# Performance work log

Hardware: AMD Instinct MI355X
Metric: run time of the kernel (lower is better)

The kernel has to match this reference:

```python
import jax, jax.numpy as jnp
import numpy as np

ND, PD, NH = 256, 128, 8   # node_dim, pair_dim, n_head
HD = ND // NH              # head_dim = 32
N, L = 1, 256


def _inorm(x):
    # InstanceNorm2d (affine=False), x is NHWC: normalize per (N,C) over H,W
    m = jnp.mean(x, axis=(1, 2), keepdims=True)
    v = jnp.var(x, axis=(1, 2), keepdims=True)
    return (x - m) * jax.lax.rsqrt(v + 1e-5)


def _conv3x3(x, w, b):
    # w in torch OIHW layout -> HWIO; stride 1, padding 1 ('SAME')
    y = jax.lax.conv_general_dilated(x, jnp.transpose(w, (2, 3, 1, 0)), (1, 1), 'SAME',
                                     dimension_numbers=('NHWC', 'HWIO', 'NHWC'))
    return y + b


def _lrelu(x):
    return jnp.where(x >= 0, x, 0.01 * x)


def _ln(x, g, b):
    m = jnp.mean(x, axis=-1, keepdims=True)
    v = jnp.var(x, axis=-1, keepdims=True)
    return (x - m) * jax.lax.rsqrt(v + 1e-5) * g + b


def setup_inputs() -> dict:
    key = jax.random.key(0)
    ks = jax.random.split(key, 16)
    rn = lambda k, s: jax.random.normal(k, s, jnp.float32) * 0.02
    return dict(
        x=jax.random.normal(ks[0], (N, L, ND), jnp.float32),
        z=jax.random.normal(ks[1], (N, L, L, PD), jnp.float32),
        plddt=jax.random.uniform(ks[2], (N, L, L, 1), jnp.float32),
        Wq=rn(ks[3], (ND, ND)), Wk=rn(ks[4], (ND, ND)), Wv=rn(ks[5], (ND, ND)),
        Wp2a=rn(ks[6], (NH, PD)),
        conv_a_w=rn(ks[7], (NH, 2 * NH, 3, 3)), conv_a_b=jnp.zeros((NH,), jnp.float32),
        conv_p_w=rn(ks[8], (NH, NH + 1, 3, 3)), conv_p_b=jnp.zeros((NH,), jnp.float32),
        ln1_g=jnp.ones((NH * PD + ND,), jnp.float32), ln1_b=jnp.zeros((NH * PD + ND,), jnp.float32),
        lin1_w=rn(ks[9], (2 * ND, NH * PD + ND)), lin1_b=jnp.zeros((2 * ND,), jnp.float32),
        ln2_g=jnp.ones((2 * ND,), jnp.float32), ln2_b=jnp.zeros((2 * ND,), jnp.float32),
        lin2_w=rn(ks[10], (ND, 2 * ND)), lin2_b=jnp.zeros((ND,), jnp.float32),
        lnf_g=jnp.ones((ND,), jnp.float32), lnf_b=jnp.zeros((ND,), jnp.float32),
        conv_z_w=rn(ks[11], (PD, NH + PD, 3, 3)), conv_z_b=jnp.zeros((PD,), jnp.float32),
    )


def reference(x, z, plddt, Wq, Wk, Wv, Wp2a, conv_a_w, conv_a_b, conv_p_w, conv_p_b,
              ln1_g, ln1_b, lin1_w, lin1_b, ln2_g, ln2_b, lin2_w, lin2_b,
              lnf_g, lnf_b, conv_z_w, conv_z_b):
    n, l, _ = x.shape
    inv_sqrt_hd = np.float32(1.0 / np.sqrt(HD))
    # _node2alpha: per-head QK^T / sqrt(head_dim) -> (N,L,L,H)
    q = (x @ Wq.T).reshape(n, l, NH, HD)
    k = (x @ Wk.T).reshape(n, l, NH, HD)
    v = (x @ Wv.T).reshape(n, l, NH, HD)
    a_node = jnp.einsum('nihd,njhd->nijh', q, k) * inv_sqrt_hd
    # _pair2alpha
    a_pair = z @ Wp2a.T  # (N,L,L,H)
    # conv2dalpha: cat(pair, node) channels-last, InstanceNorm + Conv3x3 + LeakyReLU
    alpha = _lrelu(_conv3x3(_inorm(jnp.concatenate([a_pair, a_node], axis=-1)), conv_a_w, conv_a_b))
    # alpha_mask_plddt
    alpha = _lrelu(_conv3x3(_inorm(jnp.concatenate([alpha, plddt], axis=-1)), conv_p_w, conv_p_b))
    # _node_aggregation: (N,L,H,hd) head-major flatten -> (N,L,node_dim)
    node_from_node = jnp.einsum('nijh,njhd->nihd', alpha, v).reshape(n, l, ND)
    # _pair_aggregation: direct contraction over j (avoids (N,L,L,H,P) blowup)
    node_from_pair = jnp.einsum('nijh,nijp->nihp', alpha, z).reshape(n, l, NH * PD)
    # out_transform: LN -> Linear -> LN -> LeakyReLU -> Linear
    h = jnp.concatenate([node_from_pair, node_from_node], axis=-1)
    h = _ln(h, ln1_g, ln1_b)
    h = _ln(h @ lin1_w.T + lin1_b, ln2_g, ln2_b)
    x_out = _lrelu(h) @ lin2_w.T + lin2_b
    x_new = _ln(x + x_out, lnf_g, lnf_b)
    # alpha2pair
    z_new = _lrelu(_conv3x3(_inorm(jnp.concatenate([z, alpha], axis=-1)), conv_z_w, conv_z_b))
    return x_new, z_new
```

## Files before the change

### kernel.cpp

```cpp
#include <hip/hip_runtime.h>
#include <math.h>

#define LLEN 256
#define NDIM 256
#define NHEAD 8
#define HDIM 32
#define NPIX (LLEN*LLEN)

typedef __bf16 bf16x8 __attribute__((ext_vector_type(8)));
typedef float f32x4 __attribute__((ext_vector_type(4)));

constexpr size_t OFF_Q     = 0;
constexpr size_t OFF_K     = 65536;
constexpr size_t OFF_V     = 131072;
constexpr size_t OFF_CAT16 = 196608;
constexpr size_t OFF_H1B   = 196608;
constexpr size_t OFF_W1B   = 360448;
constexpr size_t OFF_A1    = 1245184;
constexpr size_t OFF_ALPHA = 1769472;
constexpr size_t OFF_AGG   = 2293760;
constexpr size_t OFF_Y     = 2621440;
constexpr size_t OFF_ST16  = 2752512;
constexpr size_t OFF_ST9   = 2752544;
constexpr size_t OFF_ST136 = 2752576;
constexpr size_t OFF_PART  = 2752864;
constexpr size_t OFF_PART2 = 2892128;
constexpr size_t OFF_WZB2  = 3031392;

__device__ inline unsigned short f2b(float x){
  union { float f; unsigned u; } a; a.f = x;
  unsigned r = a.u + 0x7fffu + ((a.u >> 16) & 1u);
  return (unsigned short)(r >> 16);
}

__global__ __launch_bounds__(256) void qkv2_kernel(
    const float* __restrict__ x, const float* __restrict__ Wq,
    const float* __restrict__ Wk, const float* __restrict__ Wv,
    float* __restrict__ q, float* __restrict__ k, float* __restrict__ v){
  __shared__ __align__(16) float xs[4][256];
  int t = threadIdx.x;
  int i0 = blockIdx.x * 4;
  int m = blockIdx.y;
  const float* W = (m==0)?Wq:((m==1)?Wk:Wv);
  float* out = (m==0)?q:((m==1)?k:v);
  for (int idx = t; idx < 1024; idx += 256)
    xs[idx>>8][idx&255] = x[(size_t)i0*256 + idx];
  __syncthreads();
  float acc[4];
  #pragma unroll
  for (int r = 0; r < 4; r++) acc[r] = 0.f;
  const float4* wr = (const float4*)(W + (size_t)t*256);
  for (int kk = 0; kk < 64; ++kk){
    float4 w4 = wr[kk];
    #pragma unroll
    for (int r = 0; r < 4; r++){
      float4 xv = ((const float4*)xs[r])[kk];
      acc[r] += w4.x*xv.x + w4.y*xv.y + w4.z*xv.z + w4.w*xv.w;
    }
  }
  #pragma unroll
  for (int r = 0; r < 4; r++) out[(size_t)(i0+r)*256 + t] = acc[r];
}

__global__ __launch_bounds__(256) void cat16v5_kernel(
    const float* __restrict__ z, const float* __restrict__ qb,
    const float* __restrict__ kb, const float* __restrict__ Wp2a,
    float* __restrict__ cat16, float* __restrict__ p16, float* __restrict__ p16q,
    float* __restrict__ zpart, float* __restrict__ zpartq){
  __shared__ __align__(16) float zs2[32*132];
  __shared__ __align__(16) float ws2[8*132];
  __shared__ float sA[512];
  int t = threadIdx.x;
  int pix0 = blockIdx.x * 32;
  int i = pix0 >> 8;
  int j0 = pix0 & 255;
  { int h = t >> 5, j = t & 31;
    float4 v = *(const float4*)(Wp2a + h*128 + j*4);
    *(float4*)(ws2 + h*132 + j*4) = v; }
  #pragma unroll
  for (int k = 0; k < 4; ++k){
    int idx = t + k*256;
    int pix = idx >> 5, j = idx & 31;
    float4 v = *(const float4*)(z + ((size_t)(pix0 + pix))*128 + j*4);
    *(float4*)(zs2 + pix*132 + j*4) = v;
  }
  __syncthreads();
  int p8 = t >> 3, h = t & 7;
  const float* zr = zs2 + p8*132;
  const float* wr = ws2 + h*132;
  float ap = 0.f;
  #pragma unroll 8
  for (int j = 0; j < 32; ++j){
    float4 a = *(const float4*)(zr + j*4);
    float4 b = *(const float4*)(wr + j*4);
    ap += a.x*b.x + a.y*b.y + a.z*b.z + a.w*b.w;
  }
  const float* qg = qb + (size_t)i*256 + h*32;
  const float* kg = kb + (size_t)(j0 + p8)*256 + h*32;
  float an = 0.f;
  #pragma unroll
  for (int d4 = 0; d4 < 8; ++d4){
    float4 a = *(const float4*)(qg + d4*4);
    float4 b = *(const float4*)(kg + d4*4);
    an += a.x*b.x + a.y*b.y + a.z*b.z + a.w*b.w;
  }
  an *= 0.17677669529663689f;
  int pix = pix0 + p8;
  cat16[(size_t)pix*16 + h] = ap;
  cat16[(size_t)pix*16 + 8 + h] = an;
  sA[p8*16 + h] = ap;
  sA[p8*16 + 8 + h] = an;
  __syncthreads();
  if (t < 16){
    float S = 0.f, Q = 0.f;
    #pragma unroll
    for (int p = 0; p < 32; ++p){ float v = sA[p*16 + t]; S += v; Q += v*v; }
    p16 [(size_t)t*2048 + blockIdx.x] = S;
    p16q[(size_t)t*2048 + blockIdx.x] = Q;
  }
  if (t < 128){
    float S = 0.f, Q = 0.f;
    #pragma unroll 8
    for (int p = 0; p < 32; ++p){ float v = zs2[p*132 + t]; S += v; Q += v*v; }
    zpart [(size_t)t*2048 + blockIdx.x] = S;
    zpartq[(size_t)t*2048 + blockIdx.x] = Q;
  }
}

__device__ inline void block_reduce2(float& s, float& s2, float* red){
  int t = threadIdx.x;
  int lane = t & 63, wv = t >> 6;
  #pragma unroll
  for (int o = 32; o > 0; o >>= 1){ s += __shfl_down(s, o); s2 += __shfl_down(s2, o); }
  __syncthreads();
  if (lane == 0){ red[wv] = s; red[4+wv] = s2; }
  __syncthreads();
  s  = red[0]+red[1]+red[2]+red[3];
  s2 = red[4]+red[5]+red[6]+red[7];
}

__device__ inline void block_reduce2_512(float& s, float& s2, float* red16){
  int t = threadIdx.x;
  int lane = t & 63, wv = t >> 6;
  #pragma unroll
  for (int o = 32; o > 0; o >>= 1){ s += __shfl_down(s, o); s2 += __shfl_down(s2, o); }
  __syncthreads();
  if (lane == 0){ red16[wv] = s; red16[8+wv] = s2; }
  __syncthreads();
  s = 0.f; s2 = 0.f;
  #pragma unroll
  for (int j = 0; j < 8; ++j){ s += red16[j]; s2 += red16[8+j]; }
}

__global__ __launch_bounds__(256) void statsB_kernel(
    const float* __restrict__ part, const float* __restrict__ part2,
    float* __restrict__ st, int C, int co, int nb, int stride){
  __shared__ float red[8];
  int c = blockIdx.x, t = threadIdx.x;
  float s = 0.f, q = 0.f;
  for (int i = t; i < nb; i += 256){
    s += part[(size_t)c*stride + i];
    q += part2[(size_t)c*stride + i];
  }
  block_reduce2(s, q, red);
  if (t == 0){
    float m = s * (1.f/NPIX);
    float var = q * (1.f/NPIX) - m*m;
    st[co + c] = m;
    st[C + co + c] = rsqrtf(var + 1e-5f);
  }
}

__global__ __launch_bounds__(256) void statsB2_kernel(
    const float* __restrict__ p16, const float* __restrict__ p16q,
    float* __restrict__ st16,
    const float* __restrict__ zpart, const float* __restrict__ zpartq,
    float* __restrict__ st136){
  __shared__ float red[8];
  int b = blockIdx.x, t = threadIdx.x;
  const float* P; const float* Q; float* st; int C, c;
  if (b < 16){ P = p16; Q = p16q; st = st16; C = 16; c = b; }
  else       { P = zpart; Q = zpartq; st = st136; C = 136; c = b - 16; }
  float s = 0.f, q = 0.f;
  for (int i = t; i < 2048; i += 256){
    s += P[(size_t)c*2048 + i];
    q += Q[(size_t)c*2048 + i];
  }
  block_reduce2(s, q, red);
  if (t == 0){
    float m = s * (1.f/NPIX);
    float var = q * (1.f/NPIX) - m*m;
    st[c] = m;
    st[C + c] = rsqrtf(var + 1e-5f);
  }
}

template<int CIN, int COUT, bool PL>
__global__ __launch_bounds__(256) void conv_small6_kernel(
    const float* __restrict__ A, int Ca, const float* __restrict__ B, int Cb,
    const float* __restrict__ st, const float* __restrict__ w,
    const float* __restrict__ bias, float* __restrict__ out,
    const float* __restrict__ plddt, float* __restrict__ part,
    float* __restrict__ part2, int coff){
  constexpr int WD = 67;
  __shared__ float xn[3][CIN][WD];
  __shared__ float wsm[COUT*CIN*9];
  __shared__ float ms[CIN], isd[CIN], bs[COUT];
  __shared__ float sB[COUT*64];
  __shared__ float sP[64];
  int t = threadIdx.x;
  int i = blockIdx.x >> 2, chb = blockIdx.x & 3;
  int c0 = chb*64;
  if (t < CIN){ ms[t] = st[t]; isd[t] = st[CIN + t]; }
  if (t < COUT) bs[t] = bias[t];
  for (int idx = t; idx < COUT*CIN*9; idx += 256) wsm[idx] = w[idx];
  __syncthreads();
  constexpr int TOT = 66*CIN;
  for (int s = 0; s < 3; ++s){
    int ir = i - 1 + s;
    for (int idx = t; idx < TOT; idx += 256){
      int col = idx / CIN, c = idx - col*CIN;
      int gcol = c0 + col - 1;
      float vv = 0.f;
      if (ir >= 0 && ir < 256 && gcol >= 0 && gcol < 256){
        size_t pix = (size_t)ir*256 + gcol;
        float raw = (c < Ca) ? A[pix*Ca + c] : B[pix*Cb + (c - Ca)];
        vv = (raw - ms[c]) * isd[c];
      }
      xn[s][c][col] = vv;
    }
  }
  __syncthreads();
  int os = t >> 6, tc = t & 63;
  float a0 = bs[os*2], a1 = bs[os*2 + 1];
  #pragma unroll
  for (int kh = 0; kh < 3; ++kh){
    #pragma unroll
    for (int c = 0; c < CIN; ++c){
      float x0 = xn[kh][c][tc];
      float x1 = xn[kh][c][tc + 1];
      float x2 = xn[kh][c][tc + 2];
      const float* w0 = wsm + (((os*2+0)*CIN + c)*3 + kh)*3;
      const float* w1 = wsm + (((os*2+1)*CIN + c)*3 + kh)*3;
      a0 += x0*w0[0] + x1*w0[1] + x2*w0[2];
      a1 += x0*w1[0] + x1*w1[1] + x2*w1[2];
    }
  }
  a0 = (a0 >= 0.f) ? a0 : 0.01f*a0;
  a1 = (a1 >= 0.f) ? a1 : 0.01f*a1;
  float2 v2 = { a0, a1 };
  *(float2*)(out + ((size_t)(i*256 + c0 + tc))*COUT + os*2) = v2;
  sB[os*128 + tc]      = a0;
  sB[os*128 + 64 + tc] = a1;
  if (PL && t < 64) sP[t] = plddt[(size_t)i*256 + c0 + t];
  __syncthreads();
  if (t < COUT){
    int os2 = t >> 1, par = t & 1;
    const float* src = sB + os2*128 + par*64;
    float S = 0.f, Q = 0.f;
    #pragma unroll
    for (int j = 0; j < 64; ++j){ float v = src[j]; S += v; Q += v*v; }
    part [(size_t)(coff + t)*1024 + blockIdx.x] = S;
    part2[(size_t)(coff + t)*1024 + blockIdx.x] = Q;
  } else if (PL && t == COUT){
    float S = 0.f, Q = 0.f;
    #pragma unroll
    for (int j = 0; j < 64; ++j){ float v = sP[j]; S += v; Q += v*v; }
    part [(size_t)(coff + COUT)*1024 + blockIdx.x] = S;
    part2[(size_t)(coff + COUT)*1024 + blockIdx.x] = Q;
  }
}

__global__ __launch_bounds__(512) void agg_ln1_kernel(
    const float* __restrict__ alpha, const float* __restrict__ z,
    const float* __restrict__ v,
    const float* __restrict__ ln1_g, const float* __restrict__ ln1_b,
    unsigned short* __restrict__ h1b){
  __shared__ float as[2048];
  __shared__ float pp[256][4];
  __shared__ float np[256];
  __shared__ float red16[16];
  int i = blockIdx.x, t = threadIdx.x;
  for (int idx = t; idx < 2048; idx += 512) as[idx] = alpha[(size_t)i*2048 + idx];
  __syncthreads();
  int tt = t & 255, jh = t >> 8;
  int p = tt & 127, hh = tt >> 7;
  const float* zrow = z + (size_t)i*32768 + (size_t)jh*128*128;
  const float* ar0 = as + jh*128*8;
  float a0=0.f, a1=0.f, a2=0.f, a3=0.f;
  #pragma unroll 8
  for (int j = 0; j < 128; ++j){
    float zv = zrow[j*128 + p];
    const float* ar = ar0 + j*8 + hh*4;
    a0 += ar[0]*zv; a1 += ar[1]*zv; a2 += ar[2]*zv; a3 += ar[3]*zv;
  }
  int h = tt >> 5;
  float an = 0.f;
  const float* vrow = v + (size_t)jh*128*256;
  const float* ah0 = as + jh*128*8;
  #pragma unroll 8
  for (int j = 0; j < 128; ++j) an += ah0[j*8 + h]*vrow[j*256 + tt];
  if (jh == 1){
    pp[tt][0]=a0; pp[tt][1]=a1; pp[tt][2]=a2; pp[tt][3]=a3; np[tt]=an;
  }
  __syncthreads();
  float s = 0.f, s2 = 0.f;
  if (jh == 0){
    a0 += pp[tt][0]; a1 += pp[tt][1]; a2 += pp[tt][2]; a3 += pp[tt][3];
    an += np[tt];
    s  = a0 + a1 + a2 + a3 + an;
    s2 = a0*a0 + a1*a1 + a2*a2 + a3*a3 + an*an;
  }
  block_reduce2_512(s, s2, red16);
  float m = s*(1.f/1280.f), istd = rsqrtf(s2*(1.f/1280.f) - m*m + 1e-5f);
  if (jh == 0){
    size_t ob = (size_t)i*1280;
    int k0 = (hh*4+0)*128 + p;
    int k1 = (hh*4+1)*128 + p;
    int k2 = (hh*4+2)*128 + p;
    int k3 = (hh*4+3)*128 + p;
    int k4 = 1024 + tt;
    h1b[ob + k0] = f2b((a0 - m)*istd*ln1_g[k0] + ln1_b[k0]);
    h1b[ob + k1] = f2b((a1 - m)*istd*ln1_g[k1] + ln1_b[k1]);
    h1b[ob + k2] = f2b((a2 - m)*istd*ln1_g[k2] + ln1_b[k2]);
    h1b[ob + k3] = f2b((a3 - m)*istd*ln1_g[k3] + ln1_b[k3]);
    h1b[ob + k4] = f2b((an - m)*istd*ln1_g[k4] + ln1_b[k4]);
  }
}

__global__ __launch_bounds__(256) void prep_kernel(
    const float* __restrict__ lw, unsigned short* __restrict__ wb,
    const float* __restrict__ zw, unsigned short* __restrict__ wzb2){
  int bid = blockIdx.x;
  if (bid < 640){
    int idx = (bid*256 + threadIdx.x)*4;
    float4 v = *(const float4*)(lw + idx);
    ushort4 u;
    u.x = f2b(v.x); u.y = f2b(v.y); u.z = f2b(v.z); u.w = f2b(v.w);
    *(ushort4*)(wb + idx) = u;
  } else {
    int idx = (bid - 640)*256 + threadIdx.x;
    if (idx < 23040){
      int lane = idx & 63;
      int f = idx >> 6;
      int k = f % 5; int ft = f / 5; int tap = ft % 9; int ocb = ft / 9;
      int oc = ocb*16 + (lane & 15);
      int chb = k*32 + (lane >> 4)*8;
      unsigned short u[8];
      #pragma unroll
      for (int j = 0; j < 8; ++j){
        int ch = chb + j;
        float vv = (ch < 136) ? zw[(size_t)oc*1224 + ch*9 + tap] : 0.f;
        u[j] = f2b(vv);
      }
      uint4 pk;
      pk.x = (unsigned)u[0] | ((unsigned)u[1]<<16);
      pk.y = (unsigned)u[2] | ((unsigned)u[3]<<16);
      pk.z = (unsigned)u[4] | ((unsigned)u[5]<<16);
      pk.w = (unsigned)u[6] | ((unsigned)u[7]<<16);
      *(uint4*)(wzb2 + (size_t)idx*8) = pk;
    }
  }
}

__global__ __launch_bounds__(256) void gemm1_kernel(
    const unsigned short* __restrict__ h1b, const unsigned short* __restrict__ w1b,
    const float* __restrict__ lin1_b, float* __restrict__ y){
  int t = threadIdx.x;
  int mb = blockIdx.x & 3, nb = blockIdx.x >> 2;
  int lane = t & 63, w = t >> 6;
  int li = lane & 15, lg = lane >> 4;
  int mh = w & 1, nh = w >> 1;
  int mbase = mb*64 + mh*32, nbase = nb*64 + nh*32;
  f32x4 acc[2][2];
  #pragma unroll
  for (int a = 0; a < 2; ++a)
    #pragma unroll
    for (int b = 0; b < 2; ++b) acc[a][b] = (f32x4){0.f,0.f,0.f,0.f};
  const unsigned short* ar0 = h1b + (size_t)(mbase + li)*1280 + lg*8;
  const unsigned short* ar1 = ar0 + 16*1280;
  const unsigned short* br0 = w1b + (size_t)(nbase + li)*1280 + lg*8;
  const unsigned short* br1 = br0 + 16*1280;
  #pragma unroll 4
  for (int ks = 0; ks < 40; ++ks){
    bf16x8 a0 = *(const bf16x8*)(ar0 + ks*32);
    bf16x8 a1 = *(const bf16x8*)(ar1 + ks*32);
    bf16x8 b0 = *(const bf16x8*)(br0 + ks*32);
    bf16x8 b1 = *(const bf16x8*)(br1 + ks*32);
    acc[0][0] = __builtin_amdgcn_mfma_f32_16x16x32_bf16(a0, b0, acc[0][0], 0,0,0);
    acc[0][1] = __builtin_amdgcn_mfma_f32_16x16x32_bf16(a0, b1, acc[0][1], 0,0,0);
    acc[1][0] = __builtin_amdgcn_mfma_f32_16x16x32_bf16(a1, b0, acc[1][0], 0,0,0);
    acc[1][1] = __builtin_amdgcn_mfma_f32_16x16x32_bf16(a1, b1, acc[1][1], 0,0,0);
  }
  #pragma unroll
  for (int mi = 0; mi < 2; ++mi){
    #pragma unroll
    for (int ni = 0; ni < 2; ++ni){
      int col = nbase + ni*16 + li;
      float bb = lin1_b[col];
      #pragma unroll
      for (int ri = 0; ri < 4; ++ri){
        int row = mbase + mi*16 + lg*4 + ri;
        y[(size_t)row*512 + col] = acc[mi][ni][ri] + bb;
      }
    }
  }
}

__global__ __launch_bounds__(256) void outB2_kernel(
    const float* __restrict__ y, const float* __restrict__ x,
    const float* __restrict__ ln2_g, const float* __restrict__ ln2_b,
    const float* __restrict__ lin2_w, const float* __restrict__ lin2_b,
    const float* __restrict__ lnf_g, const float* __restrict__ lnf_b,
    float* __restrict__ xout){
  __shared__ __align__(16) float h2[2][512];
  __shared__ float red[8];
  int t = threadIdx.x;
  int rb = blockIdx.x;
  for (int r = 0; r < 2; ++r){
    int i = rb*2 + r;
    float y0 = y[(size_t)i*512 + t], y1 = y[(size_t)i*512 + 256 + t];
    float s = y0 + y1, s2 = y0*y0 + y1*y1;
    block_reduce2(s, s2, red);
    float m = s*(1.f/512.f), istd = rsqrtf(s2*(1.f/512.f) - m*m + 1e-5f);
    float z0 = (y0 - m)*istd*ln2_g[t] + ln2_b[t];
    float z1 = (y1 - m)*istd*ln2_g[t+256] + ln2_b[t+256];
    h2[r][t]     = (z0 >= 0.f) ? z0 : 0.01f*z0;
    h2[r][t+256] = (z1 >= 0.f) ? z1 : 0.01f*z1;
  }
  __syncthreads();
  float acc[2];
  acc[0] = 0.f; acc[1] = 0.f;
  const float4* wr = (const float4*)(lin2_w + (size_t)t*512);
  #pragma unroll 4
  for (int kk = 0; kk < 128; ++kk){
    float4 w4 = wr[kk];
    #pragma unroll
    for (int r = 0; r < 2; ++r){
      float4 h = ((const float4*)h2[r])[kk];
      acc[r] += w4.x*h.x + w4.y*h.y + w4.z*h.z + w4.w*h.w;
    }
  }
  float bb = lin2_b[t];
  for (int r = 0; r < 2; ++r){
    int i = rb*2 + r;
    float xr = x[(size_t)i*256 + t] + acc[r] + bb;
    float s = xr, s2 = xr*xr;
    block_reduce2(s, s2, red);
    float m = s*(1.f/256.f), istd = rsqrtf(s2*(1.f/256.f) - m*m + 1e-5f);
    xout[(size_t)i*256 + t] = (xr - m)*istd*lnf_g[t] + lnf_b[t];
  }
}

__global__ __launch_bounds__(256) void conv_z7_kernel(
    const float* __restrict__ z, const float* __restrict__ alpha,
    const float* __restrict__ st, const unsigned short* __restrict__ wzb2,
    const float* __restrict__ bias, float* __restrict__ out){
  __shared__ __align__(16) unsigned short xs[4*578*8];
  __shared__ float msp[153], isp[153];
  int t = threadIdx.x;
  int stripe = blockIdx.x & 7, rg = blockIdx.x >> 3;
  int i0 = rg*2, c0 = stripe*32;
  int lane = t & 63, w = t >> 6;
  int li = lane & 15, lg = lane >> 4;
  int wocb = w*2;
  if (t < 153){
    int cq = t/9, j = t - cq*9;
    bool vld = (j < 8);
    int ch = cq*8 + j;
    msp[t] = vld ? st[ch] : 0.f;
    isp[t] = vld ? st[136 + ch] : 0.f;
  }
  __syncthreads();
  for (int it = 0; it < 3; ++it){
    int cidx = t + it*256;
    int col = cidx / 17, cq = cidx - col*17;
    int gcol = c0 + col - 1;
    float mm[8], ss[8];
    #pragma unroll
    for (int j = 0; j < 8; ++j){ mm[j] = msp[cq*9 + j]; ss[j] = isp[cq*9 + j]; }
    if (cidx < 578){
      #pragma unroll
      for (int s = 0; s < 4; ++s){
        int ir = i0 - 1 + s;
        uint4 pk = {0u,0u,0u,0u};
        if (ir >= 0 && ir < 256 && gcol >= 0 && gcol < 256){
          const float* src = (cq < 16) ? (z + ((size_t)ir*256 + gcol)*128 + cq*8)
                                       : (alpha + ((size_t)ir*256 + gcol)*8);
          float4 r0 = *(const float4*)src;
          float4 r1 = *(const float4*)(src + 4);
          unsigned short u0 = f2b((r0.x - mm[0])*ss[0]);
          unsigned short u1 = f2b((r0.y - mm[1])*ss[1]);
          unsigned short u2 = f2b((r0.z - mm[2])*ss[2]);
          unsigned short u3 = f2b((r0.w - mm[3])*ss[3]);
          unsigned short u4 = f2b((r1.x - mm[4])*ss[4]);
          unsigned short u5 = f2b((r1.y - mm[5])*ss[5]);
          unsigned short u6 = f2b((r1.z - mm[6])*ss[6]);
          unsigned short u7 = f2b((r1.w - mm[7])*ss[7]);
          pk.x = (unsigned)u0 | ((unsigned)u1<<16);
          pk.y = (unsigned)u2 | ((unsigned)u3<<16);
          pk.z = (unsigned)u4 | ((unsigned)u5<<16);
          pk.w = (unsigned)u6 | ((unsigned)u7<<16);
        }
        *(uint4*)(xs + ((size_t)(s*578 + cidx))*8) = pk;
      }
    }
  }
  __syncthreads();

  f32x4 acc[2][2][2];
  #pragma unroll
  for (int r = 0; r < 2; ++r)
    #pragma unroll
    for (int m = 0; m < 2; ++m)
      #pragma unroll
      for (int o = 0; o < 2; ++o) acc[r][m][o] = (f32x4){0.f,0.f,0.f,0.f};

  for (int kh = 0; kh < 3; ++kh){
    for (int kw = 0; kw < 3; ++kw){
      int tap = kh*3 + kw;
      bf16x8 wf[5][2];
      #pragma unroll
      for (int k = 0; k < 5; ++k)
        #pragma unroll
        for (int o = 0; o < 2; ++o)
          wf[k][o] = *(const bf16x8*)(wzb2 + (size_t)((((wocb+o)*9 + tap)*5 + k)*64 + lane)*8);
      #pragma unroll
      for (int r = 0; r < 2; ++r){
        const unsigned short* sb = xs + (size_t)(r + kh)*578*8;
        #pragma unroll
        for (int k = 0; k < 5; ++k){
          int cq = (k < 4) ? (k*4 + lg) : 16;
          bf16x8 a0 = *(const bf16x8*)(sb + ((li+kw)*17 + cq)*8);
          bf16x8 a1 = *(const bf16x8*)(sb + ((li+kw+16)*17 + cq)*8);
          acc[r][0][0] = __builtin_amdgcn_mfma_f32_16x16x32_bf16(a0, wf[k][0], acc[r][0][0], 0,0,0);
          acc[r][0][1] = __builtin_amdgcn_mfma_f32_16x16x32_bf16(a0, wf[k][1], acc[r][0][1], 0,0,0);
          acc[r][1][0] = __builtin_amdgcn_mfma_f32_16x16x32_bf16(a1, wf[k][0], acc[r][1][0], 0,0,0);
          acc[r][1][1] = __builtin_amdgcn_mfma_f32_16x16x32_bf16(a1, wf[k][1], acc[r][1][1], 0,0,0);
        }
      }
    }
  }

  float b0 = bias[wocb*16 + li];
  float b1 = bias[(wocb+1)*16 + li];
  #pragma unroll
  for (int r = 0; r < 2; ++r){
    int i = i0 + r;
    #pragma unroll
    for (int m = 0; m < 2; ++m){
      #pragma unroll
      for (int ri = 0; ri < 4; ++ri){
        int px = m*16 + lg*4 + ri;
        size_t obase = ((size_t)(i*256 + c0 + px))*128;
        float v0 = acc[r][m][0][ri] + b0;
        float v1 = acc[r][m][1][ri] + b1;
        v0 = (v0 >= 0.f) ? v0 : 0.01f*v0;
        v1 = (v1 >= 0.f) ? v1 : 0.01f*v1;
        out[obase + wocb*16 + li]     = v0;
        out[obase + (wocb+1)*16 + li] = v1;
      }
    }
  }
}

extern "C" void kernel_launch(void* const* d_in, const int* in_sizes, int n_in,
                              void* d_out, int out_size, void* d_ws, size_t ws_size,
                              hipStream_t stream){
  const float* x        = (const float*)d_in[0];
  const float* z        = (const float*)d_in[1];
  const float* plddt    = (const float*)d_in[2];
  const float* Wq       = (const float*)d_in[3];
  const float* Wk       = (const float*)d_in[4];
  const float* Wv       = (const float*)d_in[5];
  const float* Wp2a     = (const float*)d_in[6];
  const float* conv_a_w = (const float*)d_in[7];
  const float* conv_a_b = (const float*)d_in[8];
  const float* conv_p_w = (const float*)d_in[9];
  const float* conv_p_b = (const float*)d_in[10];
  const float* ln1_g    = (const float*)d_in[11];
  const float* ln1_b    = (const float*)d_in[12];
  const float* lin1_w   = (const float*)d_in[13];
  const float* lin1_b   = (const float*)d_in[14];
  const float* ln2_g    = (const float*)d_in[15];
  const float* ln2_b    = (const float*)d_in[16];
  const float* lin2_w   = (const float*)d_in[17];
  const float* lin2_b   = (const float*)d_in[18];
  const float* lnf_g    = (const float*)d_in[19];
  const float* lnf_b    = (const float*)d_in[20];
  const float* conv_z_w = (const float*)d_in[21];
  const float* conv_z_b = (const float*)d_in[22];

  float* ws    = (float*)d_ws;
  float* q     = ws + OFF_Q;
  float* k     = ws + OFF_K;
  float* v     = ws + OFF_V;
  float* cat16 = ws + OFF_CAT16;
  float* a1    = ws + OFF_A1;
  float* zpart = ws + OFF_A1;
  float* zpartq= ws + OFF_A1 + 262144;
  float* alpha = ws + OFF_ALPHA;
  float* y     = ws + OFF_Y;
  float* p16   = ws + OFF_Y;
  float* p16q  = ws + OFF_Y + 32768;
  float* st16  = ws + OFF_ST16;
  float* st9   = ws + OFF_ST9;
  float* st136 = ws + OFF_ST136;
  float* part  = ws + OFF_PART;
  float* part2 = ws + OFF_PART2;
  unsigned short* wzb2 = (unsigned short*)(ws + OFF_WZB2);
  unsigned short* h1b  = (unsigned short*)(ws + OFF_H1B);
  unsigned short* w1b  = (unsigned short*)(ws + OFF_W1B);

  float* xout = (float*)d_out;
  float* zout = (float*)d_out + 65536;

  qkv2_kernel<<<dim3(64,3), 256, 0, stream>>>(x, Wq, Wk, Wv, q, k, v);
  cat16v5_kernel<<<2048, 256, 0, stream>>>(z, q, k, Wp2a, cat16, p16, p16q,
                                           zpart, zpartq);
  statsB2_kernel<<<144, 256, 0, stream>>>(p16, p16q, st16, zpart, zpartq, st136);
  conv_small6_kernel<16,8,true><<<1024, 256, 0, stream>>>(
      cat16, 16, (const float*)nullptr, 0, st16, conv_a_w, conv_a_b, a1,
      plddt, part, part2, 0);
  statsB_kernel<<<9, 256, 0, stream>>>(part, part2, st9, 9, 0, 1024, 1024);
  conv_small6_kernel<9,8,false><<<1024, 256, 0, stream>>>(
      a1, 8, plddt, 1, st9, conv_p_w, conv_p_b, alpha,
      (const float*)nullptr, part, part2, 128);
  statsB_kernel<<<8, 256, 0, stream>>>(part + (size_t)128*1024,
                                       part2 + (size_t)128*1024,
                                       st136, 136, 128, 1024, 1024);
  agg_ln1_kernel<<<256, 512, 0, stream>>>(alpha, z, v, ln1_g, ln1_b, h1b);
  prep_kernel<<<730, 256, 0, stream>>>(lin1_w, w1b, conv_z_w, wzb2);
  gemm1_kernel<<<32, 256, 0, stream>>>(h1b, w1b, lin1_b, y);
  outB2_kernel<<<128, 256, 0, stream>>>(y, x, ln2_g, ln2_b, lin2_w, lin2_b,
                                        lnf_g, lnf_b, xout);
  conv_z7_kernel<<<1024, 256, 0, stream>>>(z, alpha, st136, wzb2, conv_z_b, zout);
}
```

Measured before the change: 175.1 us.

## Fuse lin1 GEMM with LN2, lin2 and final LN into one kernel

```diff
diff --git a/kernel.cpp b/kernel.cpp
--- a/kernel.cpp
+++ b/kernel.cpp
@@ -18,7 +18,6 @@
 constexpr size_t OFF_W1B   = 360448;
 constexpr size_t OFF_A1    = 1245184;
 constexpr size_t OFF_ALPHA = 1769472;
-constexpr size_t OFF_AGG   = 2293760;
 constexpr size_t OFF_Y     = 2621440;
 constexpr size_t OFF_ST16  = 2752512;
 constexpr size_t OFF_ST9   = 2752544;
@@ -363,88 +362,73 @@
   }
 }
 
-__global__ __launch_bounds__(256) void gemm1_kernel(
+__global__ __launch_bounds__(256) void out_fused_kernel(
     const unsigned short* __restrict__ h1b, const unsigned short* __restrict__ w1b,
-    const float* __restrict__ lin1_b, float* __restrict__ y){
-  int t = threadIdx.x;
-  int mb = blockIdx.x & 3, nb = blockIdx.x >> 2;
-  int lane = t & 63, w = t >> 6;
-  int li = lane & 15, lg = lane >> 4;
-  int mh = w & 1, nh = w >> 1;
-  int mbase = mb*64 + mh*32, nbase = nb*64 + nh*32;
-  f32x4 acc[2][2];
-  #pragma unroll
-  for (int a = 0; a < 2; ++a)
-    #pragma unroll
-    for (int b = 0; b < 2; ++b) acc[a][b] = (f32x4){0.f,0.f,0.f,0.f};
-  const unsigned short* ar0 = h1b + (size_t)(mbase + li)*1280 + lg*8;
-  const unsigned short* ar1 = ar0 + 16*1280;
-  const unsigned short* br0 = w1b + (size_t)(nbase + li)*1280 + lg*8;
-  const unsigned short* br1 = br0 + 16*1280;
-  #pragma unroll 4
-  for (int ks = 0; ks < 40; ++ks){
-    bf16x8 a0 = *(const bf16x8*)(ar0 + ks*32);
-    bf16x8 a1 = *(const bf16x8*)(ar1 + ks*32);
-    bf16x8 b0 = *(const bf16x8*)(br0 + ks*32);
-    bf16x8 b1 = *(const bf16x8*)(br1 + ks*32);
-    acc[0][0] = __builtin_amdgcn_mfma_f32_16x16x32_bf16(a0, b0, acc[0][0], 0,0,0);
-    acc[0][1] = __builtin_amdgcn_mfma_f32_16x16x32_bf16(a0, b1, acc[0][1], 0,0,0);
-    acc[1][0] = __builtin_amdgcn_mfma_f32_16x16x32_bf16(a1, b0, acc[1][0], 0,0,0);
-    acc[1][1] = __builtin_amdgcn_mfma_f32_16x16x32_bf16(a1, b1, acc[1][1], 0,0,0);
-  }
-  #pragma unroll
-  for (int mi = 0; mi < 2; ++mi){
-    #pragma unroll
-    for (int ni = 0; ni < 2; ++ni){
-      int col = nbase + ni*16 + li;
-      float bb = lin1_b[col];
-      #pragma unroll
-      for (int ri = 0; ri < 4; ++ri){
-        int row = mbase + mi*16 + lg*4 + ri;
-        y[(size_t)row*512 + col] = acc[mi][ni][ri] + bb;
-      }
-    }
-  }
-}
-
-__global__ __launch_bounds__(256) void outB2_kernel(
-    const float* __restrict__ y, const float* __restrict__ x,
+    const float* __restrict__ lin1_b, const float* __restrict__ x,
     const float* __restrict__ ln2_g, const float* __restrict__ ln2_b,
     const float* __restrict__ lin2_w, const float* __restrict__ lin2_b,
     const float* __restrict__ lnf_g, const float* __restrict__ lnf_b,
     float* __restrict__ xout){
-  __shared__ __align__(16) float h2[2][512];
+  __shared__ __align__(16) float yl[8][512];
   __shared__ float red[8];
   int t = threadIdx.x;
-  int rb = blockIdx.x;
-  for (int r = 0; r < 2; ++r){
-    int i = rb*2 + r;
-    float y0 = y[(size_t)i*512 + t], y1 = y[(size_t)i*512 + 256 + t];
+  int i0 = blockIdx.x * 8;
+  int lane = t & 63, w = t >> 6;
+  int li = lane & 15, lg = lane >> 4;
+  int arow = i0 + li; if (arow > 255) arow = 255;
+  f32x4 acc[8];
+  #pragma unroll
+  for (int n = 0; n < 8; ++n) acc[n] = (f32x4){0.f,0.f,0.f,0.f};
+  const unsigned short* ar = h1b + (size_t)arow*1280 + lg*8;
+  #pragma unroll 4
+  for (int ks = 0; ks < 40; ++ks){
+    bf16x8 a = *(const bf16x8*)(ar + ks*32);
+    #pragma unroll
+    for (int n = 0; n < 8; ++n){
+      const unsigned short* br = w1b + (size_t)(w*128 + n*16 + li)*1280 + ks*32 + lg*8;
+      bf16x8 b = *(const bf16x8*)br;
+      acc[n] = __builtin_amdgcn_mfma_f32_16x16x32_bf16(a, b, acc[n], 0,0,0);
+    }
+  }
+  #pragma unroll
+  for (int n = 0; n < 8; ++n){
+    int col = w*128 + n*16 + li;
+    float bb = lin1_b[col];
+    #pragma unroll
+    for (int ri = 0; ri < 4; ++ri){
+      int dr = lg*4 + ri;
+      if (dr < 8) yl[dr][col] = acc[n][ri] + bb;
+    }
+  }
+  __syncthreads();
+  for (int r = 0; r < 8; ++r){
+    float y0 = yl[r][t], y1 = yl[r][t + 256];
     float s = y0 + y1, s2 = y0*y0 + y1*y1;
     block_reduce2(s, s2, red);
     float m = s*(1.f/512.f), istd = rsqrtf(s2*(1.f/512.f) - m*m + 1e-5f);
     float z0 = (y0 - m)*istd*ln2_g[t] + ln2_b[t];
     float z1 = (y1 - m)*istd*ln2_g[t+256] + ln2_b[t+256];
-    h2[r][t]     = (z0 >= 0.f) ? z0 : 0.01f*z0;
-    h2[r][t+256] = (z1 >= 0.f) ? z1 : 0.01f*z1;
-  }
-  __syncthreads();
-  float acc[2];
-  acc[0] = 0.f; acc[1] = 0.f;
-  const float4* wr = (const float4*)(lin2_w + (size_t)t*512);
+    yl[r][t]     = (z0 >= 0.f) ? z0 : 0.01f*z0;
+    yl[r][t+256] = (z1 >= 0.f) ? z1 : 0.01f*z1;
+    __syncthreads();
+  }
+  float a8[8];
+  #pragma unroll
+  for (int r = 0; r < 8; ++r) a8[r] = 0.f;
+  const float4* wr2 = (const float4*)(lin2_w + (size_t)t*512);
   #pragma unroll 4
   for (int kk = 0; kk < 128; ++kk){
-    float4 w4 = wr[kk];
-    #pragma unroll
-    for (int r = 0; r < 2; ++r){
-      float4 h = ((const float4*)h2[r])[kk];
-      acc[r] += w4.x*h.x + w4.y*h.y + w4.z*h.z + w4.w*h.w;
-    }
-  }
-  float bb = lin2_b[t];
-  for (int r = 0; r < 2; ++r){
-    int i = rb*2 + r;
-    float xr = x[(size_t)i*256 + t] + acc[r] + bb;
+    float4 w4 = wr2[kk];
+    #pragma unroll
+    for (int r = 0; r < 8; ++r){
+      float4 h = *(const float4*)(&yl[r][kk*4]);
+      a8[r] += w4.x*h.x + w4.y*h.y + w4.z*h.z + w4.w*h.w;
+    }
+  }
+  float bb2 = lin2_b[t];
+  for (int r = 0; r < 8; ++r){
+    int i = i0 + r;
+    float xr = x[(size_t)i*256 + t] + a8[r] + bb2;
     float s = xr, s2 = xr*xr;
     block_reduce2(s, s2, red);
     float m = s*(1.f/256.f), istd = rsqrtf(s2*(1.f/256.f) - m*m + 1e-5f);
@@ -600,7 +584,6 @@
   float* zpart = ws + OFF_A1;
   float* zpartq= ws + OFF_A1 + 262144;
   float* alpha = ws + OFF_ALPHA;
-  float* y     = ws + OFF_Y;
   float* p16   = ws + OFF_Y;
   float* p16q  = ws + OFF_Y + 32768;
   float* st16  = ws + OFF_ST16;
@@ -631,8 +614,8 @@
                                        st136, 136, 128, 1024, 1024);
   agg_ln1_kernel<<<256, 512, 0, stream>>>(alpha, z, v, ln1_g, ln1_b, h1b);
   prep_kernel<<<730, 256, 0, stream>>>(lin1_w, w1b, conv_z_w, wzb2);
-  gemm1_kernel<<<32, 256, 0, stream>>>(h1b, w1b, lin1_b, y);
-  outB2_kernel<<<128, 256, 0, stream>>>(y, x, ln2_g, ln2_b, lin2_w, lin2_b,
-                                        lnf_g, lnf_b, xout);
+  out_fused_kernel<<<32, 256, 0, stream>>>(h1b, w1b, lin1_b, x,
+                                           ln2_g, ln2_b, lin2_w, lin2_b,
+                                           lnf_g, lnf_b, xout);
   conv_z7_kernel<<<1024, 256, 0, stream>>>(z, alpha, st136, wzb2, conv_z_b, zout);
 }
```

Result: slower. 224.0 us (+27.9%).
